# Performance work log

Hardware: AMD Instinct MI355X
Metric: run time of the kernel (lower is better)

## Reference

```python
import jax, jax.numpy as jnp
import numpy as np

N_NODES = 50000


def _segment_mean(vals, seg_ids, num_segments):
    s = jax.ops.segment_sum(vals, seg_ids, num_segments=num_segments)
    cnt = jax.ops.segment_sum(jnp.ones((vals.shape[0],), vals.dtype), seg_ids,
                              num_segments=num_segments)
    return s / jnp.clip(cnt, 1.0)[:, None]


def _sage_layer(h, src, dst, W_self, W_neigh, b):
    # mean-aggregate neighbor messages: gather h[src], scatter-mean to dst
    neigh = _segment_mean(h[src], dst, N_NODES)
    return h @ W_self + neigh @ W_neigh + b


def _edge_score(h, src, dst, Wp, bp):
    # concat(h_u, h_v) @ Wp == h_u @ Wp[:d] + h_v @ Wp[d:]
    d = h.shape[1]
    return h[src] @ Wp[:d] + h[dst] @ Wp[d:] + bp


def setup_inputs() -> dict:
    key = jax.random.key(0)
    ks = jax.random.split(key, 16)
    N, E, EP, EN = N_NODES, 800000, 200000, 200000
    d_in, d_hid, d_out = 128, 256, 128
    inp = {
        'x': jax.random.normal(ks[0], (N, d_in), jnp.float32),
        'msg_src': jax.random.randint(ks[1], (E,), 0, N, jnp.int32),
        'msg_dst': jax.random.randint(ks[2], (E,), 0, N, jnp.int32),
        'pos_src': jax.random.randint(ks[3], (EP,), 0, N, jnp.int32),
        'pos_dst': jax.random.randint(ks[4], (EP,), 0, N, jnp.int32),
        'neg_src': jax.random.randint(ks[5], (EN,), 0, N, jnp.int32),
        'neg_dst': jax.random.randint(ks[6], (EN,), 0, N, jnp.int32),
        'W1_self': jax.random.normal(ks[7], (d_in, d_hid), jnp.float32) * 0.05,
        'W1_neigh': jax.random.normal(ks[8], (d_in, d_hid), jnp.float32) * 0.05,
        'b1': jnp.zeros((d_hid,), jnp.float32),
        'W2_self': jax.random.normal(ks[9], (d_hid, d_out), jnp.float32) * 0.05,
        'W2_neigh': jax.random.normal(ks[10], (d_hid, d_out), jnp.float32) * 0.05,
        'b2': jnp.zeros((d_out,), jnp.float32),
        'Wp': jax.random.normal(ks[11], (2 * d_out, 1), jnp.float32) * 0.05,
        'bp': jnp.zeros((1,), jnp.float32),
    }
    return inp


def reference(x, msg_src, msg_dst, pos_src, pos_dst, neg_src, neg_dst,
              W1_self, W1_neigh, b1, W2_self, W2_neigh, b2, Wp, bp):
    h = _sage_layer(x, msg_src, msg_dst, W1_self, W1_neigh, b1)
    h = jax.nn.relu(h)
    h = _sage_layer(h, msg_src, msg_dst, W2_self, W2_neigh, b2)
    pos_score = _edge_score(h, pos_src, pos_dst, Wp, bp)
    neg_score = _edge_score(h, neg_src, neg_dst, Wp, bp)
    return pos_score, neg_score
```

## Files before the change

### kernel.cpp

```cpp
#include <hip/hip_runtime.h>


#define NN 50000
#define EM 800000
#define EPOS 200000
#define ENEG 200000
#define NB 196
#define CAP 8192
#define RPB 4096
#define CBLK 196
#define MTILES 3125
#define GEMM_GRID 512
#define XCONV 6250
#define BT 1024

typedef __bf16 bf16;
typedef bf16 bf16x4 __attribute__((ext_vector_type(4)));
typedef bf16 bf16x8 __attribute__((ext_vector_type(8)));
typedef float floatx4 __attribute__((ext_vector_type(4)));

#define I_CNT  0
#define I_OFF  38416
#define I_ROW  76832
#define I_REND 127008
#define I_CSR  177184
#define B_CREG 7131264
#define B_XB   10331264
#define B_AGG1 23131264
#define B_H1   35931264
#define B_NV   61531264
#define B_WT1  62331264
#define B_WT2  62462336
#define B_P    62593408
#define B_Q    62793408

__global__ __launch_bounds__(256) void convbin_kernel(
    const float* __restrict__ x, bf16* __restrict__ xb,
    const float* __restrict__ W1s, const float* __restrict__ W1n,
    const float* __restrict__ W2n, const float* __restrict__ W2s,
    bf16* __restrict__ Wt1, bf16* __restrict__ Wt2,
    const int* __restrict__ msrc, const int* __restrict__ mdst,
    unsigned* __restrict__ creg, int* __restrict__ cntM,
    int* __restrict__ offM) {
    if (blockIdx.x < XCONV) {
        int i = blockIdx.x * 256 + threadIdx.x;
        float4 v = ((const float4*)x)[i];
        bf16x4 o;
        o[0] = (bf16)v.x; o[1] = (bf16)v.y; o[2] = (bf16)v.z; o[3] = (bf16)v.w;
        *(bf16x4*)(xb + (size_t)i * 4) = o;
    } else if (blockIdx.x < XCONV + 256) {
        int i = (blockIdx.x - XCONV) * 256 + threadIdx.x;
        int n = i >> 8, k = i & 255;
        float w1 = (k < 128) ? W1s[k * 256 + n] : W1n[(k - 128) * 256 + n];
        Wt1[i] = (bf16)w1;
        float w2 = (n < 128) ? W2n[k * 128 + n] : W2s[k * 128 + (n - 128)];
        Wt2[i] = (bf16)w2;
    } else {
        __shared__ int hist[NB];
        __shared__ int cnt2[NB];
        __shared__ int base[256];
        __shared__ unsigned sorted[RPB];
        int t = threadIdx.x;
        int cb = blockIdx.x - (XCONV + 256);
        int e0 = cb * RPB;
        int nrec = EM - e0; if (nrec > RPB) nrec = RPB;

        for (int i = t; i < NB; i += 256) { hist[i] = 0; cnt2[i] = 0; }
        __syncthreads();

        int myb[16];
        unsigned myrec[16];
#pragma unroll
        for (int j = 0; j < 16; ++j) {
            int idx = j * 256 + t;
            if (idx < nrec) {
                int s = msrc[e0 + idx], d = mdst[e0 + idx];
                myb[j] = d >> 8;
                myrec[j] = ((unsigned)(d & 255) << 16) | (unsigned)s;
                atomicAdd(&hist[myb[j]], 1);
            } else myb[j] = -1;
        }
        __syncthreads();

        base[t] = (t < NB) ? hist[t] : 0;
        __syncthreads();
        for (int o = 1; o < 256; o <<= 1) {
            int u = (t >= o) ? base[t - o] : 0;
            __syncthreads();
            base[t] += u;
            __syncthreads();
        }

#pragma unroll
        for (int j = 0; j < 16; ++j) {
            if (myb[j] >= 0) {
                int rk = atomicAdd(&cnt2[myb[j]], 1);
                int slot = base[myb[j]] - hist[myb[j]] + rk;
                sorted[slot] = myrec[j];
            }
        }
        __syncthreads();

        if (t < NB) {
            cntM[t * CBLK + cb] = hist[t];
            offM[t * CBLK + cb] = base[t] - hist[t];
        }
#pragma unroll
        for (int j = 0; j < 16; ++j) {
            int idx = j * 256 + t;
            if (idx < nrec) creg[(size_t)cb * RPB + idx] = sorted[idx];
        }
    }
}

__global__ __launch_bounds__(1024) void bucket_kernel(
    const unsigned* __restrict__ creg, const int* __restrict__ cntM,
    const int* __restrict__ offM, int* __restrict__ rowstart,
    int* __restrict__ rowend, int* __restrict__ csr,
    const bf16* __restrict__ feat, bf16* __restrict__ agg) {
    __shared__ unsigned lrec[CAP];
    __shared__ unsigned lsrc[CAP];
    __shared__ int ccnt[256];
    __shared__ int cpos[256];
    __shared__ int coff[256];
    __shared__ int lhist[256];
    __shared__ int sc[256];
    __shared__ int lcur[256];
    int b = blockIdx.x, t = threadIdx.x;

    if (t < 256) {
        int cc = 0, oo = 0;
        if (t < CBLK) { cc = cntM[b * CBLK + t]; oo = offM[b * CBLK + t]; }
        ccnt[t] = cc; cpos[t] = cc; coff[t] = oo; lhist[t] = 0;
    }
    __syncthreads();
    for (int o = 1; o < 256; o <<= 1) {
        int u = (t < 256 && t >= o) ? cpos[t - o] : 0;
        __syncthreads();
        if (t < 256) cpos[t] += u;
        __syncthreads();
    }

    int wid = t >> 6, lane = t & 63;
    for (int cb = wid; cb < CBLK; cb += 16) {
        int c = ccnt[cb], ofs = coff[cb], d0 = cpos[cb] - c;
        for (int i = lane; i < c; i += 64) {
            unsigned rec = creg[(size_t)cb * RPB + ofs + i];
            lrec[d0 + i] = rec;
            atomicAdd(&lhist[(int)(rec >> 16) & 255], 1);
        }
    }
    __syncthreads();
    int cntb = cpos[255];

    if (t < 256) sc[t] = lhist[t];
    __syncthreads();
    for (int o = 1; o < 256; o <<= 1) {
        int u = (t < 256 && t >= o) ? sc[t - o] : 0;
        __syncthreads();
        if (t < 256) sc[t] += u;
        __syncthreads();
    }
    if (t < 256) {
        int node = b * 256 + t;
        if (node < NN) {
            rowstart[node] = b * CAP + sc[t] - lhist[t];
            rowend[node] = b * CAP + sc[t];
        }
        lcur[t] = sc[t] - lhist[t];
    }
    __syncthreads();

    for (int i = t; i < cntb; i += BT) {
        unsigned rec = lrec[i];
        int slot = atomicAdd(&lcur[(int)(rec >> 16) & 255], 1);
        lsrc[slot] = rec & 0xffffu;
    }
    __syncthreads();
    for (int i = t; i < cntb; i += BT) csr[b * CAP + i] = (int)lsrc[i];

    int q = lane >> 4, r = lane & 15;
    int cch = r * 8;
    for (int k = 0; k < 16; ++k) {
        int ln = wid * 16 + k;
        int node = b * 256 + ln;
        if (node >= NN) break;
        int beg = sc[ln] - lhist[ln], end = sc[ln];
        float acc[8] = {0.f, 0.f, 0.f, 0.f, 0.f, 0.f, 0.f, 0.f};
        float acc2[8] = {0.f, 0.f, 0.f, 0.f, 0.f, 0.f, 0.f, 0.f};
        int i = beg + q;
        for (; i + 4 < end; i += 8) {
            int s0 = (int)lsrc[i], s1 = (int)lsrc[i + 4];
            bf16x8 v0 = *(const bf16x8*)(feat + (size_t)s0 * 128 + cch);
            bf16x8 v1 = *(const bf16x8*)(feat + (size_t)s1 * 128 + cch);
#pragma unroll
            for (int u = 0; u < 8; ++u) {
                acc[u] += (float)v0[u];
                acc2[u] += (float)v1[u];
            }
        }
        if (i < end) {
            int s0 = (int)lsrc[i];
            bf16x8 v0 = *(const bf16x8*)(feat + (size_t)s0 * 128 + cch);
#pragma unroll
            for (int u = 0; u < 8; ++u) acc[u] += (float)v0[u];
        }
#pragma unroll
        for (int u = 0; u < 8; ++u) acc[u] += acc2[u];
#pragma unroll
        for (int m = 16; m <= 32; m <<= 1)
#pragma unroll
            for (int u = 0; u < 8; ++u) acc[u] += __shfl_xor(acc[u], m);
        if (q == 0) {
            int deg = end - beg;
            float inv = 1.0f / (float)(deg > 0 ? deg : 1);
            bf16x8 o;
#pragma unroll
            for (int u = 0; u < 8; ++u) o[u] = (bf16)(acc[u] * inv);
            *(bf16x8*)(agg + (size_t)node * 128 + cch) = o;
        }
    }
}

__global__ __launch_bounds__(256) void gemm1_kernel(
    const bf16* __restrict__ xb, const bf16* __restrict__ aggb,
    const bf16* __restrict__ Wt, const float* __restrict__ b1,
    bf16* __restrict__ h1b) {
    int w = threadIdx.x >> 6;
    int lane = threadIdx.x & 63;
    int r = lane & 15, quad = lane >> 4;
    int colbase = w * 64;

    bf16x8 bfr[4][8];
#pragma unroll
    for (int t = 0; t < 4; ++t)
#pragma unroll
        for (int kk = 0; kk < 8; ++kk)
            bfr[t][kk] = *(const bf16x8*)(Wt + (size_t)(colbase + t * 16 + r) * 256
                                          + kk * 32 + quad * 8);
    float bb[4];
#pragma unroll
    for (int t = 0; t < 4; ++t) bb[t] = b1[colbase + t * 16 + r];

    for (int tile = blockIdx.x; tile < MTILES; tile += GEMM_GRID) {
        int m0 = tile * 16;
        int row = m0 + r;
        bf16x8 a[8];
#pragma unroll
        for (int kk = 0; kk < 4; ++kk)
            a[kk] = *(const bf16x8*)(xb + (size_t)row * 128 + kk * 32 + quad * 8);
#pragma unroll
        for (int kk = 4; kk < 8; ++kk)
            a[kk] = *(const bf16x8*)(aggb + (size_t)row * 128 + (kk - 4) * 32 + quad * 8);
        floatx4 acc[4];
#pragma unroll
        for (int t = 0; t < 4; ++t) acc[t] = (floatx4){0.f, 0.f, 0.f, 0.f};
#pragma unroll
        for (int kk = 0; kk < 8; ++kk)
#pragma unroll
            for (int t = 0; t < 4; ++t)
                acc[t] = __builtin_amdgcn_mfma_f32_16x16x32_bf16(a[kk], bfr[t][kk],
                                                                 acc[t], 0, 0, 0);
        int mb = m0 + quad * 4;
#pragma unroll
        for (int t = 0; t < 4; ++t) {
            int col = colbase + t * 16 + r;
#pragma unroll
            for (int rr = 0; rr < 4; ++rr) {
                float v = acc[t][rr] + bb[t];
                v = v > 0.f ? v : 0.f;
                h1b[(size_t)(mb + rr) * 256 + col] = (bf16)v;
            }
        }
    }
}

__global__ __launch_bounds__(256) void gemm2_kernel(
    const bf16* __restrict__ h1b, const bf16* __restrict__ Wt,
    const float* __restrict__ b2, const float* __restrict__ wp,
    float4* __restrict__ nodev) {
    __shared__ float lp[4][16];
    __shared__ float lq[4][16];
    int w = threadIdx.x >> 6;
    int lane = threadIdx.x & 63;
    int r = lane & 15, quad = lane >> 4;
    int colbase = w * 64;

    bf16x8 bfr[4][8];
#pragma unroll
    for (int t = 0; t < 4; ++t)
#pragma unroll
        for (int kk = 0; kk < 8; ++kk)
            bfr[t][kk] = *(const bf16x8*)(Wt + (size_t)(colbase + t * 16 + r) * 256
                                          + kk * 32 + quad * 8);
    float bb[4], wA[4], wB[4];
#pragma unroll
    for (int t = 0; t < 4; ++t) {
        int col = colbase + t * 16 + r;
        if (w < 2) {
            bb[t] = 0.f;
            wA[t] = wp[col];
            wB[t] = wp[128 + col];
        } else {
            int c2 = col - 128;
            bb[t] = b2[c2];
            wA[t] = wp[c2];
            wB[t] = wp[128 + c2];
        }
    }

    for (int tile = blockIdx.x; tile < MTILES; tile += GEMM_GRID) {
        int m0 = tile * 16;
        int row = m0 + r;
        bf16x8 a[8];
#pragma unroll
        for (int kk = 0; kk < 8; ++kk)
            a[kk] = *(const bf16x8*)(h1b + (size_t)row * 256 + kk * 32 + quad * 8);
        floatx4 acc[4];
#pragma unroll
        for (int t = 0; t < 4; ++t) acc[t] = (floatx4){0.f, 0.f, 0.f, 0.f};
#pragma unroll
        for (int kk = 0; kk < 8; ++kk)
#pragma unroll
            for (int t = 0; t < 4; ++t)
                acc[t] = __builtin_amdgcn_mfma_f32_16x16x32_bf16(a[kk], bfr[t][kk],
                                                                 acc[t], 0, 0, 0);
        float pacc[4], qacc[4];
#pragma unroll
        for (int rr = 0; rr < 4; ++rr) {
            float pr = 0.f, qr = 0.f;
#pragma unroll
            for (int t = 0; t < 4; ++t) {
                float v = acc[t][rr] + bb[t];
                pr += v * wA[t];
                qr += v * wB[t];
            }
            pacc[rr] = pr;
            qacc[rr] = qr;
        }
#pragma unroll
        for (int m = 1; m <= 8; m <<= 1) {
#pragma unroll
            for (int rr = 0; rr < 4; ++rr) {
                pacc[rr] += __shfl_xor(pacc[rr], m);
                qacc[rr] += __shfl_xor(qacc[rr], m);
            }
        }
        if (r == 0) {
#pragma unroll
            for (int rr = 0; rr < 4; ++rr) {
                lp[w][quad * 4 + rr] = pacc[rr];
                lq[w][quad * 4 + rr] = qacc[rr];
            }
        }
        __syncthreads();
        if (threadIdx.x < 16) {
            int rw = threadIdx.x;
            float4 o;
            o.x = lp[0][rw] + lp[1][rw];
            o.y = lq[0][rw] + lq[1][rw];
            o.z = lp[2][rw] + lp[3][rw];
            o.w = lq[2][rw] + lq[3][rw];
            nodev[m0 + rw] = o;
        }
        __syncthreads();
    }
}

__global__ __launch_bounds__(256) void gather2_kernel(
    const float4* __restrict__ nodev, const int* __restrict__ rowstart,
    const int* __restrict__ rowend, const int* __restrict__ csr,
    float* __restrict__ p, float* __restrict__ q) {
    int t = threadIdx.x;
    int node = blockIdx.x * 16 + (t >> 4);
    if (node >= NN) return;
    int l = t & 15;
    int beg = rowstart[node], end = rowend[node];
    float pz = 0.f, qz = 0.f;
    for (int i = beg + l; i < end; i += 16) {
        float4 v = nodev[csr[i]];
        pz += v.x;
        qz += v.y;
    }
#pragma unroll
    for (int m = 8; m >= 1; m >>= 1) {
        pz += __shfl_xor(pz, m);
        qz += __shfl_xor(qz, m);
    }
    if (l == 0) {
        int deg = end - beg;
        float inv = 1.0f / (float)(deg > 0 ? deg : 1);
        float4 me = nodev[node];
        p[node] = me.z + pz * inv;
        q[node] = me.w + qz * inv;
    }
}

__global__ __launch_bounds__(256) void score_kernel(
    const int* __restrict__ psrc, const int* __restrict__ pdst,
    const int* __restrict__ nsrc, const int* __restrict__ ndst,
    const float* __restrict__ p, const float* __restrict__ q,
    const float* __restrict__ bp, float* __restrict__ out) {
    int i = blockIdx.x * blockDim.x + threadIdx.x;
    float b = bp[0];
    if (i < EPOS) {
        out[i] = p[psrc[i]] + q[pdst[i]] + b;
    } else if (i < EPOS + ENEG) {
        int j = i - EPOS;
        out[i] = p[nsrc[j]] + q[ndst[j]] + b;
    }
}

extern "C" void kernel_launch(void* const* d_in, const int* in_sizes, int n_in,
                              void* d_out, int out_size, void* d_ws, size_t ws_size,
                              hipStream_t stream) {
    const float* x    = (const float*)d_in[0];
    const int*   msrc = (const int*)d_in[1];
    const int*   mdst = (const int*)d_in[2];
    const int*   psrc = (const int*)d_in[3];
    const int*   pdst = (const int*)d_in[4];
    const int*   nsrc = (const int*)d_in[5];
    const int*   ndst = (const int*)d_in[6];
    const float* W1s  = (const float*)d_in[7];
    const float* W1n  = (const float*)d_in[8];
    const float* b1   = (const float*)d_in[9];
    const float* W2s  = (const float*)d_in[10];
    const float* W2n  = (const float*)d_in[11];
    const float* b2   = (const float*)d_in[12];
    const float* wp   = (const float*)d_in[13];
    const float* bp   = (const float*)d_in[14];

    char* ws = (char*)d_ws;
    int*   cntM     = (int*)ws + I_CNT;
    int*   offM     = (int*)ws + I_OFF;
    int*   rowstart = (int*)ws + I_ROW;
    int*   rowend   = (int*)ws + I_REND;
    int*   csr      = (int*)ws + I_CSR;
    unsigned* creg  = (unsigned*)(ws + B_CREG);
    bf16*  xb    = (bf16*)(ws + B_XB);
    bf16*  agg1b = (bf16*)(ws + B_AGG1);
    bf16*  h1b   = (bf16*)(ws + B_H1);
    float4* nodev = (float4*)(ws + B_NV);
    bf16*  Wt1   = (bf16*)(ws + B_WT1);
    bf16*  Wt2   = (bf16*)(ws + B_WT2);
    float* p     = (float*)(ws + B_P);
    float* q     = (float*)(ws + B_Q);
    float* out   = (float*)d_out;

    convbin_kernel<<<XCONV + 256 + CBLK, 256, 0, stream>>>(
        x, xb, W1s, W1n, W2n, W2s, Wt1, Wt2, msrc, mdst, creg, cntM, offM);
    bucket_kernel<<<NB, BT, 0, stream>>>(creg, cntM, offM, rowstart, rowend,
                                         csr, xb, agg1b);
    gemm1_kernel<<<GEMM_GRID, 256, 0, stream>>>(xb, agg1b, Wt1, b1, h1b);
    gemm2_kernel<<<GEMM_GRID, 256, 0, stream>>>(h1b, Wt2, b2, wp, nodev);
    gather2_kernel<<<(NN + 15) / 16, 256, 0, stream>>>(nodev, rowstart, rowend, csr, p, q);
    score_kernel<<<(EPOS + ENEG + 255) / 256, 256, 0, stream>>>(
        psrc, pdst, nsrc, ndst, p, q, bp, out);
}
```

Baseline: 215.2 us.

## Split bucket sort from layer-1 gather into separate high-occupancy kernel

The layer-1 neighbor mean aggregation is moved out of the 196-block bucket/sort kernel into its own kernel with one wavefront per node across about 12500 blocks, reading CSR indices from global memory. The inner loop is unrolled four ways so more independent gathers are in flight. The aim is to stop the irregular gather being limited to 196 workgroups, which leaves most CUs idle. The GEMM grid size is also doubled. The cost is an extra kernel launch and reading CSR and row bounds back from global memory rather than LDS.

```diff
diff --git a/kernel.cpp b/kernel.cpp
--- a/kernel.cpp
+++ b/kernel.cpp
@@ -10,7 +10,7 @@
 #define RPB 4096
 #define CBLK 196
 #define MTILES 3125
-#define GEMM_GRID 512
+#define GEMM_GRID 1024
 #define XCONV 6250
 #define BT 1024
 
@@ -113,11 +113,10 @@
     }
 }
 
-__global__ __launch_bounds__(1024) void bucket_kernel(
+__global__ __launch_bounds__(1024) void bsort_kernel(
     const unsigned* __restrict__ creg, const int* __restrict__ cntM,
     const int* __restrict__ offM, int* __restrict__ rowstart,
-    int* __restrict__ rowend, int* __restrict__ csr,
-    const bf16* __restrict__ feat, bf16* __restrict__ agg) {
+    int* __restrict__ rowend, int* __restrict__ csr) {
     __shared__ unsigned lrec[CAP];
     __shared__ unsigned lsrc[CAP];
     __shared__ int ccnt[256];
@@ -178,47 +177,57 @@
     }
     __syncthreads();
     for (int i = t; i < cntb; i += BT) csr[b * CAP + i] = (int)lsrc[i];
-
+}
+
+__global__ __launch_bounds__(256) void gather1_kernel(const bf16* __restrict__ feat,
+                                                      const int* __restrict__ rowstart,
+                                                      const int* __restrict__ rowend,
+                                                      const int* __restrict__ csr,
+                                                      bf16* __restrict__ agg) {
+    int node = (blockIdx.x * 256 + threadIdx.x) >> 6;
+    if (node >= NN) return;
+    int lane = threadIdx.x & 63;
     int q = lane >> 4, r = lane & 15;
-    int cch = r * 8;
-    for (int k = 0; k < 16; ++k) {
-        int ln = wid * 16 + k;
-        int node = b * 256 + ln;
-        if (node >= NN) break;
-        int beg = sc[ln] - lhist[ln], end = sc[ln];
-        float acc[8] = {0.f, 0.f, 0.f, 0.f, 0.f, 0.f, 0.f, 0.f};
-        float acc2[8] = {0.f, 0.f, 0.f, 0.f, 0.f, 0.f, 0.f, 0.f};
-        int i = beg + q;
-        for (; i + 4 < end; i += 8) {
-            int s0 = (int)lsrc[i], s1 = (int)lsrc[i + 4];
-            bf16x8 v0 = *(const bf16x8*)(feat + (size_t)s0 * 128 + cch);
-            bf16x8 v1 = *(const bf16x8*)(feat + (size_t)s1 * 128 + cch);
-#pragma unroll
-            for (int u = 0; u < 8; ++u) {
-                acc[u] += (float)v0[u];
-                acc2[u] += (float)v1[u];
-            }
-        }
-        if (i < end) {
-            int s0 = (int)lsrc[i];
-            bf16x8 v0 = *(const bf16x8*)(feat + (size_t)s0 * 128 + cch);
-#pragma unroll
-            for (int u = 0; u < 8; ++u) acc[u] += (float)v0[u];
-        }
-#pragma unroll
-        for (int u = 0; u < 8; ++u) acc[u] += acc2[u];
-#pragma unroll
-        for (int m = 16; m <= 32; m <<= 1)
-#pragma unroll
-            for (int u = 0; u < 8; ++u) acc[u] += __shfl_xor(acc[u], m);
-        if (q == 0) {
-            int deg = end - beg;
-            float inv = 1.0f / (float)(deg > 0 ? deg : 1);
-            bf16x8 o;
-#pragma unroll
-            for (int u = 0; u < 8; ++u) o[u] = (bf16)(acc[u] * inv);
-            *(bf16x8*)(agg + (size_t)node * 128 + cch) = o;
-        }
+    int c = r * 8;
+    int beg = rowstart[node], end = rowend[node];
+    float a0[8] = {0.f, 0.f, 0.f, 0.f, 0.f, 0.f, 0.f, 0.f};
+    float a1[8] = {0.f, 0.f, 0.f, 0.f, 0.f, 0.f, 0.f, 0.f};
+    float a2[8] = {0.f, 0.f, 0.f, 0.f, 0.f, 0.f, 0.f, 0.f};
+    float a3[8] = {0.f, 0.f, 0.f, 0.f, 0.f, 0.f, 0.f, 0.f};
+    int i = beg + q;
+    for (; i + 12 < end; i += 16) {
+        int s0 = csr[i], s1 = csr[i + 4], s2 = csr[i + 8], s3 = csr[i + 12];
+        bf16x8 v0 = *(const bf16x8*)(feat + (size_t)s0 * 128 + c);
+        bf16x8 v1 = *(const bf16x8*)(feat + (size_t)s1 * 128 + c);
+        bf16x8 v2 = *(const bf16x8*)(feat + (size_t)s2 * 128 + c);
+        bf16x8 v3 = *(const bf16x8*)(feat + (size_t)s3 * 128 + c);
+#pragma unroll
+        for (int u = 0; u < 8; ++u) {
+            a0[u] += (float)v0[u];
+            a1[u] += (float)v1[u];
+            a2[u] += (float)v2[u];
+            a3[u] += (float)v3[u];
+        }
+    }
+    for (; i < end; i += 4) {
+        int s0 = csr[i];
+        bf16x8 v0 = *(const bf16x8*)(feat + (size_t)s0 * 128 + c);
+#pragma unroll
+        for (int u = 0; u < 8; ++u) a0[u] += (float)v0[u];
+    }
+#pragma unroll
+    for (int u = 0; u < 8; ++u) a0[u] += a1[u] + a2[u] + a3[u];
+#pragma unroll
+    for (int m = 16; m <= 32; m <<= 1)
+#pragma unroll
+        for (int u = 0; u < 8; ++u) a0[u] += __shfl_xor(a0[u], m);
+    if (q == 0) {
+        int deg = end - beg;
+        float inv = 1.0f / (float)(deg > 0 ? deg : 1);
+        bf16x8 o;
+#pragma unroll
+        for (int u = 0; u < 8; ++u) o[u] = (bf16)(a0[u] * inv);
+        *(bf16x8*)(agg + (size_t)node * 128 + c) = o;
     }
 }
 
@@ -449,8 +458,8 @@
 
     convbin_kernel<<<XCONV + 256 + CBLK, 256, 0, stream>>>(
         x, xb, W1s, W1n, W2n, W2s, Wt1, Wt2, msrc, mdst, creg, cntM, offM);
-    bucket_kernel<<<NB, BT, 0, stream>>>(creg, cntM, offM, rowstart, rowend,
-                                         csr, xb, agg1b);
+    bsort_kernel<<<NB, BT, 0, stream>>>(creg, cntM, offM, rowstart, rowend, csr);
+    gather1_kernel<<<(NN + 3) / 4, 256, 0, stream>>>(xb, rowstart, rowend, csr, agg1b);
     gemm1_kernel<<<GEMM_GRID, 256, 0, stream>>>(xb, agg1b, Wt1, b1, h1b);
     gemm2_kernel<<<GEMM_GRID, 256, 0, stream>>>(h1b, Wt2, b2, wp, nodev);
     gather2_kernel<<<(NN + 15) / 16, 256, 0, stream>>>(nodev, rowstart, rowend, csr, p, q);
```

Result: slower. 233.2 us (+8.4%).
